# Performance work log

Measured on AMD Instinct MI355X. Metric: run time of the kernel, lower is better.

Reference implementation:

```python
import jax, jax.numpy as jnp
from jax import lax
import numpy as np

HPDF = np.array([-0.0544158422, 0.3128715909, -0.6756307363, 0.5853546837,
                 0.0158291053, -0.284015543, -0.0004724846, 0.1287474266,
                 0.017369301, -0.0440882539, -0.0139810279, 0.008746094,
                 0.004870353, -0.0003917404, -0.0006754494, -0.0001174768],
                dtype=np.float32)


def setup_inputs() -> dict:
    key = jax.random.key(0)
    x = jax.random.normal(key, (8, 3, 512, 512), dtype=jnp.float32)
    hpdf = jnp.asarray(HPDF)
    return {"x": x, "hpdf": hpdf}


def _dwconv(inp, k2d, channels):
    # depthwise valid cross-correlation (matches F.conv2d with groups=C)
    n = k2d.shape[0]
    k = jnp.broadcast_to(k2d[None, None], (channels, 1, n, n))
    return lax.conv_general_dilated(
        inp, k, window_strides=(1, 1), padding='VALID',
        dimension_numbers=('NCHW', 'OIHW', 'NCHW'),
        feature_group_count=channels)


def reference(x, hpdf):
    B, C, H, W = x.shape
    n = hpdf.shape[0]  # 16 taps
    sign = (-1.0) ** jnp.arange(n, dtype=jnp.float32)
    lpdf = sign * hpdf[::-1]
    filters = [jnp.outer(lpdf, hpdf),   # LH
               jnp.outer(hpdf, lpdf),   # HL
               jnp.outer(hpdf, hpdf)]   # HH
    pad = n - 1  # 15
    xp = jnp.pad(x, ((0, 0), (0, 0), (pad, pad), (pad, pad)), mode='reflect')

    xis = []
    for f in filters:
        R = _dwconv(xp, f, C)                       # [B,C,H+15,W+15]
        xi = _dwconv(jnp.abs(R), jnp.abs(f[::-1, ::-1]), C)  # [B,C,H,W]
        # filter side length 16 is even -> roll by 1 on both spatial dims
        xi = jnp.roll(jnp.roll(xi, 1, axis=-1), 1, axis=-2)
        xis.append(xi)

    xi_stack = jnp.stack(xis, axis=0)               # [3,B,C,H,W]
    # p = -1: rho = (sum xi^p)^(-1/p) = sum(1/xi)
    rho = jnp.sum(1.0 / xi_stack, axis=0)
    wet = 1e10
    rho = jnp.minimum(rho, wet)
    rho = jnp.where(jnp.isnan(rho), wet, rho)
    mn = rho.min(axis=(-2, -1), keepdims=True)
    mx = rho.max(axis=(-2, -1), keepdims=True)
    rho = (rho - mn) / (mx - mn + 1e-8)
    score = jax.nn.sigmoid(1.0 - rho)
    return x * score
```

## Files before the change

### kernel.cpp

```cpp
#include <hip/hip_runtime.h>
#include <math.h>

#define IMG   512
#define NIMG  24
#define XST   72
#define TST   104
#define RST   56
#define UST   88
#define UOFF  4480
#define P1SZ  7296
#define TSZ   (48 * TST)

typedef _Float16 v8h __attribute__((ext_vector_type(8)));
typedef float    v4f __attribute__((ext_vector_type(4)));

__device__ __forceinline__ v8h load8(const _Float16* p) {
    union { uint4 u; v8h h; } c;
    c.u = *(const uint4*)p;
    return c.h;
}

__device__ __forceinline__ void store4(_Float16* p, v4f a) {
    union { _Float16 h[4]; uint2 u; } c;
    c.h[0] = (_Float16)a[0]; c.h[1] = (_Float16)a[1];
    c.h[2] = (_Float16)a[2]; c.h[3] = (_Float16)a[3];
    *(uint2*)p = c.u;
}

__device__ __forceinline__ void store4abs(_Float16* p, v4f a) {
    union { _Float16 h[4]; uint2 u; } c;
    c.h[0] = (_Float16)fabsf(a[0]); c.h[1] = (_Float16)fabsf(a[1]);
    c.h[2] = (_Float16)fabsf(a[2]); c.h[3] = (_Float16)fabsf(a[3]);
    *(uint2*)p = c.u;
}

__device__ __forceinline__ unsigned pkrtz(float a, float b) {
    union { __fp16 __attribute__((ext_vector_type(2))) v; unsigned u; } c;
    c.v = __builtin_amdgcn_cvt_pkrtz(a, b);
    return c.u;
}

__device__ __forceinline__ unsigned short f2bf(float f) {
    unsigned b = __float_as_uint(f);
    b = (b + 0x7fffu + ((b >> 16) & 1u)) >> 16;
    return (unsigned short)b;
}

__device__ __forceinline__ int refl(int g) {
    return g < 0 ? -g : (g >= IMG ? 2 * IMG - 2 - g : g);
}

__global__ __launch_bounds__(512, 6) void stego_stage1(
    const float* __restrict__ x, const float* __restrict__ hpdf,
    unsigned short* __restrict__ rho_out, float2* __restrict__ bmm)
{
    __shared__ __align__(16) _Float16 pool1[P1SZ];
    __shared__ __align__(16) _Float16 sTL[TSZ];
    __shared__ __align__(16) _Float16 sTH[TSZ];
    __shared__ __align__(16) _Float16 btab[256];
    __shared__ float red[16];

    const int tid = threadIdx.x;
    const int lane = tid & 63, wid = tid >> 6;
    const int n16 = lane & 15, quad = lane >> 4;
    const int Oj = blockIdx.x * 32, Oi = blockIdx.y * 64, img = blockIdx.z;
    const float* ximg = x + (size_t)img * IMG * IMG;

    if (tid < 256) {
        int mode = tid >> 6, t = tid & 63;
        float v = 0.f;
        if (t >= 16 && t < 32) {
            int tap = t - 16;
            int idx = (mode == 0 || mode == 2) ? tap : 15 - tap;
            float c = hpdf[idx];
            if (mode == 1 && (tap & 1)) c = -c;
            if (mode >= 2) c = fabsf(c);
            v = c;
        }
        btab[tid] = (_Float16)v;
    }

    {
        const int cp2 = tid & 31, row0 = tid >> 5;
        const int c0 = Oj - 15 + 2 * cp2;
        if (Oi >= 15 && Oi <= 433 && Oj >= 15 && Oj <= 463) {
            const float* src = ximg + (size_t)(Oi - 15) * IMG + c0;
            #pragma unroll
            for (int k = 0; k < 6; ++k) {
                int i = row0 + (k << 4);
                unsigned pv = 0;
                if (i < 94) pv = pkrtz(src[(size_t)i * IMG], src[(size_t)i * IMG + 1]);
                *(unsigned*)(pool1 + i * XST + 2 * cp2) = pv;
            }
        } else {
            int gj0 = refl(c0), gj1 = refl(c0 + 1);
            #pragma unroll
            for (int k = 0; k < 6; ++k) {
                int i = row0 + (k << 4);
                unsigned pv = 0;
                if (i < 94) {
                    int gi = refl(Oi - 15 + i);
                    pv = pkrtz(ximg[gi * IMG + gj0], ximg[gi * IMG + gj1]);
                }
                *(unsigned*)(pool1 + i * XST + 2 * cp2) = pv;
            }
        }
    }
    __syncthreads();

    v8h band[4];
    {
        const int boff = 16 + quad * 8 - n16;
        #pragma unroll
        for (int m = 0; m < 4; ++m)
            #pragma unroll
            for (int j = 0; j < 8; ++j)
                band[m][j] = btab[m * 64 + boff + j];
    }

    for (int u = wid; u < 18; u += 8) {
        int mt = u % 6, nt = u / 6;
        int m0 = mt * 16, n0 = nt * 16;
        v8h a = load8(pool1 + (m0 + n16) * XST + n0 + quad * 8);
        v4f z = {0.f, 0.f, 0.f, 0.f};
        v4f cL = __builtin_amdgcn_mfma_f32_16x16x32_f16(a, band[1], z, 0, 0, 0);
        v4f cH = __builtin_amdgcn_mfma_f32_16x16x32_f16(a, band[0], z, 0, 0, 0);
        int off = (n0 + n16) * TST + m0 + quad * 4;
        store4(sTL + off, cL);
        store4(sTH + off, cH);
    }
    __syncthreads();

    float rho[4] = {0.f, 0.f, 0.f, 0.f};
    _Float16* Rb = pool1;
    _Float16* Ub = pool1 + UOFF;

    const int fB[3] = {0, 1, 0};
    const int fC[3] = {2, 3, 3};
    const int fD[3] = {3, 2, 3};

    #pragma unroll
    for (int f = 0; f < 3; ++f) {
        const _Float16* Tsrc = (f == 0) ? sTL : sTH;

        for (int u = wid; u < 15; u += 8) {
            int nt = u % 5, mt = u / 5;
            int i0 = nt * 16, c0 = mt * 16;
            v8h a = load8(Tsrc + (c0 + n16) * TST + i0 + quad * 8);
            v4f z = {0.f, 0.f, 0.f, 0.f};
            v4f acc = __builtin_amdgcn_mfma_f32_16x16x32_f16(a, band[fB[f]], z, 0, 0, 0);
            store4abs(Rb + (i0 + n16) * RST + c0 + quad * 4, acc);
        }
        __syncthreads();

        for (int u = wid; u < 10; u += 8) {
            int mt = u % 5, nt = u / 5;
            int i0 = mt * 16, j0 = nt * 16;
            v8h a = load8(Rb + (i0 + n16) * RST + j0 + quad * 8);
            v4f z = {0.f, 0.f, 0.f, 0.f};
            v4f acc = __builtin_amdgcn_mfma_f32_16x16x32_f16(a, band[fC[f]], z, 0, 0, 0);
            store4(Ub + (j0 + n16) * UST + i0 + quad * 4, acc);
        }
        __syncthreads();

        {
            int i0 = (wid & 3) * 16, c0 = (wid >> 2) * 16;
            v8h a = load8(Ub + (c0 + n16) * UST + i0 + quad * 8);
            v4f z = {0.f, 0.f, 0.f, 0.f};
            v4f acc = __builtin_amdgcn_mfma_f32_16x16x32_f16(a, band[fD[f]], z, 0, 0, 0);
            #pragma unroll
            for (int r = 0; r < 4; ++r) rho[r] += __builtin_amdgcn_rcpf(acc[r]);
        }
    }

    const size_t rbase = (size_t)img * (IMG * IMG);
    const int i_out = (Oi + (wid & 3) * 16 + n16 + 1) & 511;
    const int c0f = (wid >> 2) * 16;
    float lmin = 1e38f, lmax = 0.f;
    #pragma unroll
    for (int r = 0; r < 4; ++r) {
        float v = rho[r];
        v = isnan(v) ? 1e10f : fminf(v, 1e10f);
        unsigned short b = f2bf(v);
        int j_out = (Oj + c0f + quad * 4 + r + 1) & 511;
        rho_out[rbase + ((size_t)i_out << 9) + j_out] = b;
        float rq = __uint_as_float((unsigned)b << 16);
        lmin = fminf(lmin, rq);
        lmax = fmaxf(lmax, rq);
    }
    #pragma unroll
    for (int off = 32; off >= 1; off >>= 1) {
        lmin = fminf(lmin, __shfl_xor(lmin, off));
        lmax = fmaxf(lmax, __shfl_xor(lmax, off));
    }
    if ((tid & 63) == 0) { red[wid] = lmin; red[8 + wid] = lmax; }
    __syncthreads();
    if (tid == 0) {
        float m0 = red[0], m1 = red[8];
        #pragma unroll
        for (int k = 1; k < 8; ++k) { m0 = fminf(m0, red[k]); m1 = fmaxf(m1, red[8 + k]); }
        bmm[(img << 7) + blockIdx.y * 16 + blockIdx.x] = make_float2(m0, m1);
    }
}

__global__ __launch_bounds__(256) void stego_stage2(
    const float* __restrict__ x, const unsigned short* __restrict__ rho,
    const float2* __restrict__ bmm, float* __restrict__ out)
{
    __shared__ float sred[8];
    const int tid = threadIdx.x;
    const int t = blockIdx.x * 256 + tid;
    const int img = t >> 15;

    float lmn = 1e38f, lmx = 0.f;
    if (tid < 128) { float2 p = bmm[(img << 7) + tid]; lmn = p.x; lmx = p.y; }
    #pragma unroll
    for (int off = 32; off >= 1; off >>= 1) {
        lmn = fminf(lmn, __shfl_xor(lmn, off));
        lmx = fmaxf(lmx, __shfl_xor(lmx, off));
    }
    if (tid < 128 && (tid & 63) == 0) { sred[tid >> 6] = lmn; sred[4 + (tid >> 6)] = lmx; }
    __syncthreads();
    const float mn = fminf(sred[0], sred[1]);
    const float mx = fmaxf(sred[4], sred[5]);
    const float inv = __builtin_amdgcn_rcpf(mx - mn + 1e-8f);

    const size_t base = (size_t)t << 3;
    uint4 rb = *(const uint4*)(rho + base);
    unsigned ru[4] = {rb.x, rb.y, rb.z, rb.w};
    float r[8];
    #pragma unroll
    for (int k = 0; k < 4; ++k) {
        r[2 * k]     = __uint_as_float(ru[k] << 16);
        r[2 * k + 1] = __uint_as_float(ru[k] & 0xffff0000u);
    }

    const float* xrow = x + base;
    float4 xa = *(const float4*)xrow;
    float4 xb = *(const float4*)(xrow + 4);
    float xs[8] = {xa.x, xa.y, xa.z, xa.w, xb.x, xb.y, xb.z, xb.w};
    float os[8];
    #pragma unroll
    for (int k = 0; k < 8; ++k) {
        float rn = (r[k] - mn) * inv;
        os[k] = xs[k] * __builtin_amdgcn_rcpf(1.f + __expf(rn - 1.f));
    }
    float* orow = out + base;
    *(float4*)orow       = make_float4(os[0], os[1], os[2], os[3]);
    *(float4*)(orow + 4) = make_float4(os[4], os[5], os[6], os[7]);
}

extern "C" void kernel_launch(void* const* d_in, const int* in_sizes, int n_in,
                              void* d_out, int out_size, void* d_ws, size_t ws_size,
                              hipStream_t stream) {
    const float* x    = (const float*)d_in[0];
    const float* hpdf = (const float*)d_in[1];
    float* out = (float*)d_out;

    unsigned short* rho = (unsigned short*)d_ws;
    float2* bmm = (float2*)((char*)d_ws + (size_t)NIMG * IMG * IMG * 2);

    hipLaunchKernelGGL(stego_stage1, dim3(IMG / 32, IMG / 64, NIMG), dim3(512), 0, stream,
                       x, hpdf, rho, bmm);
    const int total8 = NIMG * IMG * IMG / 8;
    hipLaunchKernelGGL(stego_stage2, dim3(total8 / 256), dim3(256), 0, stream,
                       x, rho, bmm, out);
}
```

Measured before the change: 119.7 us.

## Vectorize tile loads, store rho unrolled, and map images to XCDs

The input tile load now reads float4 per thread with a one-column shift, which is compensated by alternate band coefficient vectors (bandA). Rho is written in natural order as packed 8-byte stores, and the roll by one is moved into stage 2 through a row offset plus a lane shuffle. Both kernels use a 1D grid remapped so each image's blocks land on the same XCD, which should improve L2 locality. The index remapping and shifted filter coefficients are easy to get subtly wrong.

```diff
diff --git a/kernel.cpp b/kernel.cpp
--- a/kernel.cpp
+++ b/kernel.cpp
@@ -20,6 +20,12 @@
     return c.h;
 }
 
+__device__ __forceinline__ unsigned pkrtz(float a, float b) {
+    union { __fp16 __attribute__((ext_vector_type(2))) v; unsigned u; } c;
+    c.v = __builtin_amdgcn_cvt_pkrtz(a, b);
+    return c.u;
+}
+
 __device__ __forceinline__ void store4(_Float16* p, v4f a) {
     union { _Float16 h[4]; uint2 u; } c;
     c.h[0] = (_Float16)a[0]; c.h[1] = (_Float16)a[1];
@@ -32,12 +38,6 @@
     c.h[0] = (_Float16)fabsf(a[0]); c.h[1] = (_Float16)fabsf(a[1]);
     c.h[2] = (_Float16)fabsf(a[2]); c.h[3] = (_Float16)fabsf(a[3]);
     *(uint2*)p = c.u;
-}
-
-__device__ __forceinline__ unsigned pkrtz(float a, float b) {
-    union { __fp16 __attribute__((ext_vector_type(2))) v; unsigned u; } c;
-    c.v = __builtin_amdgcn_cvt_pkrtz(a, b);
-    return c.u;
 }
 
 __device__ __forceinline__ unsigned short f2bf(float f) {
@@ -57,17 +57,25 @@
     __shared__ __align__(16) _Float16 pool1[P1SZ];
     __shared__ __align__(16) _Float16 sTL[TSZ];
     __shared__ __align__(16) _Float16 sTH[TSZ];
-    __shared__ __align__(16) _Float16 btab[256];
+    __shared__ __align__(16) _Float16 btab[512];
     __shared__ float red[16];
 
     const int tid = threadIdx.x;
-    const int lane = tid & 63, wid = tid >> 6;
+    const int lane = tid & 63;
+    const int wid = __builtin_amdgcn_readfirstlane(tid >> 6);
     const int n16 = lane & 15, quad = lane >> 4;
-    const int Oj = blockIdx.x * 32, Oi = blockIdx.y * 64, img = blockIdx.z;
-    const float* ximg = x + (size_t)img * IMG * IMG;
-
-    if (tid < 256) {
-        int mode = tid >> 6, t = tid & 63;
+
+    const int blk = blockIdx.x;
+    const int xcd = blk & 7;
+    const int grp = blk >> 3;
+    const int img = xcd + ((grp >> 7) << 3);
+    const int tl  = grp & 127;
+    const int Oi = (tl >> 4) << 6;
+    const int Oj = (tl & 15) << 5;
+    const float* ximg = x + (size_t)img * (IMG * IMG);
+
+    {
+        const int mode = tid >> 7, t = tid & 127;
         float v = 0.f;
         if (t >= 16 && t < 32) {
             int tap = t - 16;
@@ -81,41 +89,54 @@
     }
 
     {
-        const int cp2 = tid & 31, row0 = tid >> 5;
-        const int c0 = Oj - 15 + 2 * cp2;
-        if (Oi >= 15 && Oi <= 433 && Oj >= 15 && Oj <= 463) {
-            const float* src = ximg + (size_t)(Oi - 15) * IMG + c0;
-            #pragma unroll
-            for (int k = 0; k < 6; ++k) {
-                int i = row0 + (k << 4);
-                unsigned pv = 0;
-                if (i < 94) pv = pkrtz(src[(size_t)i * IMG], src[(size_t)i * IMG + 1]);
-                *(unsigned*)(pool1 + i * XST + 2 * cp2) = pv;
+        const int cg = tid & 15, row0 = tid >> 4;
+        const int c0 = Oj - 16 + 4 * cg;
+        _Float16* dst = pool1 + row0 * XST + 4 * cg;
+        if (Oi >= 15 && Oi <= 433 && Oj >= 16 && Oj <= 464) {
+            const float* src = ximg + (size_t)(Oi - 15 + row0) * IMG + c0;
+            #pragma unroll
+            for (int k = 0; k < 3; ++k) {
+                const int row = row0 + (k << 5);
+                uint2 pv = make_uint2(0u, 0u);
+                if (row < 94) {
+                    float4 xv = *(const float4*)(src + (size_t)(k << 5) * IMG);
+                    pv.x = pkrtz(xv.x, xv.y);
+                    pv.y = pkrtz(xv.z, xv.w);
+                }
+                *(uint2*)(dst + (size_t)(k << 5) * XST) = pv;
             }
         } else {
-            int gj0 = refl(c0), gj1 = refl(c0 + 1);
-            #pragma unroll
-            for (int k = 0; k < 6; ++k) {
-                int i = row0 + (k << 4);
-                unsigned pv = 0;
-                if (i < 94) {
-                    int gi = refl(Oi - 15 + i);
-                    pv = pkrtz(ximg[gi * IMG + gj0], ximg[gi * IMG + gj1]);
+            const int gj0 = refl(c0),     gj1 = refl(c0 + 1);
+            const int gj2 = refl(c0 + 2), gj3 = refl(c0 + 3);
+            #pragma unroll
+            for (int k = 0; k < 3; ++k) {
+                const int row = row0 + (k << 5);
+                uint2 pv = make_uint2(0u, 0u);
+                if (row < 94) {
+                    const float* rsrc = ximg + (size_t)refl(Oi - 15 + row) * IMG;
+                    pv.x = pkrtz(rsrc[gj0], rsrc[gj1]);
+                    pv.y = pkrtz(rsrc[gj2], rsrc[gj3]);
                 }
-                *(unsigned*)(pool1 + i * XST + 2 * cp2) = pv;
+                *(uint2*)(dst + (size_t)(k << 5) * XST) = pv;
             }
         }
     }
     __syncthreads();
 
-    v8h band[4];
+    v8h band[4], bandA[2];
     {
-        const int boff = 16 + quad * 8 - n16;
+        const int boff  = 16 + quad * 8 - n16;
+        const int boffA = 15 + quad * 8 - n16;
         #pragma unroll
         for (int m = 0; m < 4; ++m)
             #pragma unroll
             for (int j = 0; j < 8; ++j)
-                band[m][j] = btab[m * 64 + boff + j];
+                band[m][j] = btab[m * 128 + boff + j];
+        #pragma unroll
+        for (int m = 0; m < 2; ++m)
+            #pragma unroll
+            for (int j = 0; j < 8; ++j)
+                bandA[m][j] = btab[m * 128 + boffA + j];
     }
 
     for (int u = wid; u < 18; u += 8) {
@@ -123,8 +144,8 @@
         int m0 = mt * 16, n0 = nt * 16;
         v8h a = load8(pool1 + (m0 + n16) * XST + n0 + quad * 8);
         v4f z = {0.f, 0.f, 0.f, 0.f};
-        v4f cL = __builtin_amdgcn_mfma_f32_16x16x32_f16(a, band[1], z, 0, 0, 0);
-        v4f cH = __builtin_amdgcn_mfma_f32_16x16x32_f16(a, band[0], z, 0, 0, 0);
+        v4f cL = __builtin_amdgcn_mfma_f32_16x16x32_f16(a, bandA[1], z, 0, 0, 0);
+        v4f cH = __builtin_amdgcn_mfma_f32_16x16x32_f16(a, bandA[0], z, 0, 0, 0);
         int off = (n0 + n16) * TST + m0 + quad * 4;
         store4(sTL + off, cL);
         store4(sTH + off, cH);
@@ -174,20 +195,26 @@
     }
 
     const size_t rbase = (size_t)img * (IMG * IMG);
-    const int i_out = (Oi + (wid & 3) * 16 + n16 + 1) & 511;
-    const int c0f = (wid >> 2) * 16;
+    const int i_nat = Oi + (wid & 3) * 16 + n16;
+    const int jb = Oj + ((wid >> 2) << 4) + quad * 4;
     float lmin = 1e38f, lmax = 0.f;
-    #pragma unroll
-    for (int r = 0; r < 4; ++r) {
-        float v = rho[r];
-        v = isnan(v) ? 1e10f : fminf(v, 1e10f);
-        unsigned short b = f2bf(v);
-        int j_out = (Oj + c0f + quad * 4 + r + 1) & 511;
-        rho_out[rbase + ((size_t)i_out << 9) + j_out] = b;
-        float rq = __uint_as_float((unsigned)b << 16);
-        lmin = fminf(lmin, rq);
-        lmax = fmaxf(lmax, rq);
-    }
+    unsigned pk0, pk1;
+    {
+        unsigned short b[4];
+        #pragma unroll
+        for (int r = 0; r < 4; ++r) {
+            float v = rho[r];
+            v = isnan(v) ? 1e10f : fminf(v, 1e10f);
+            b[r] = f2bf(v);
+            float rq = __uint_as_float((unsigned)b[r] << 16);
+            lmin = fminf(lmin, rq);
+            lmax = fmaxf(lmax, rq);
+        }
+        pk0 = (unsigned)b[0] | ((unsigned)b[1] << 16);
+        pk1 = (unsigned)b[2] | ((unsigned)b[3] << 16);
+    }
+    *(uint2*)(rho_out + rbase + ((size_t)i_nat << 9) + jb) = make_uint2(pk0, pk1);
+
     #pragma unroll
     for (int off = 32; off >= 1; off >>= 1) {
         lmin = fminf(lmin, __shfl_xor(lmin, off));
@@ -199,7 +226,7 @@
         float m0 = red[0], m1 = red[8];
         #pragma unroll
         for (int k = 1; k < 8; ++k) { m0 = fminf(m0, red[k]); m1 = fmaxf(m1, red[8 + k]); }
-        bmm[(img << 7) + blockIdx.y * 16 + blockIdx.x] = make_float2(m0, m1);
+        bmm[(img << 7) + tl] = make_float2(m0, m1);
     }
 }
 
@@ -209,8 +236,13 @@
 {
     __shared__ float sred[8];
     const int tid = threadIdx.x;
-    const int t = blockIdx.x * 256 + tid;
-    const int img = t >> 15;
+    const int lane = tid & 63;
+
+    const int blk = blockIdx.x;
+    const int xcd = blk & 7, grp = blk >> 3;
+    const int img = xcd + ((grp >> 7) << 3);
+    const int chunk = grp & 127;
+    const int t = (img << 15) + (chunk << 8) + tid;
 
     float lmn = 1e38f, lmx = 0.f;
     if (tid < 128) { float2 p = bmm[(img << 7) + tid]; lmn = p.x; lmx = p.y; }
@@ -225,16 +257,23 @@
     const float mx = fmaxf(sred[4], sred[5]);
     const float inv = __builtin_amdgcn_rcpf(mx - mn + 1e-8f);
 
+    const int i = (t >> 6) & 511;
+    const int rrow = (i - 1) & 511;
+    const size_t rb_off = ((size_t)img << 18) + ((size_t)rrow << 9) + ((size_t)lane << 3);
+    uint4 rb = *(const uint4*)(rho + rb_off);
+    unsigned ru[4] = {rb.x, rb.y, rb.z, rb.w};
+    float f7 = __uint_as_float(ru[3] & 0xffff0000u);
+    float r[8];
+    r[0] = __shfl(f7, (lane + 63) & 63);
+    r[1] = __uint_as_float(ru[0] << 16);
+    r[2] = __uint_as_float(ru[0] & 0xffff0000u);
+    r[3] = __uint_as_float(ru[1] << 16);
+    r[4] = __uint_as_float(ru[1] & 0xffff0000u);
+    r[5] = __uint_as_float(ru[2] << 16);
+    r[6] = __uint_as_float(ru[2] & 0xffff0000u);
+    r[7] = __uint_as_float(ru[3] << 16);
+
     const size_t base = (size_t)t << 3;
-    uint4 rb = *(const uint4*)(rho + base);
-    unsigned ru[4] = {rb.x, rb.y, rb.z, rb.w};
-    float r[8];
-    #pragma unroll
-    for (int k = 0; k < 4; ++k) {
-        r[2 * k]     = __uint_as_float(ru[k] << 16);
-        r[2 * k + 1] = __uint_as_float(ru[k] & 0xffff0000u);
-    }
-
     const float* xrow = x + base;
     float4 xa = *(const float4*)xrow;
     float4 xb = *(const float4*)(xrow + 4);
@@ -260,9 +299,8 @@
     unsigned short* rho = (unsigned short*)d_ws;
     float2* bmm = (float2*)((char*)d_ws + (size_t)NIMG * IMG * IMG * 2);
 
-    hipLaunchKernelGGL(stego_stage1, dim3(IMG / 32, IMG / 64, NIMG), dim3(512), 0, stream,
+    hipLaunchKernelGGL(stego_stage1, dim3(NIMG * 128), dim3(512), 0, stream,
                        x, hpdf, rho, bmm);
-    const int total8 = NIMG * IMG * IMG / 8;
-    hipLaunchKernelGGL(stego_stage2, dim3(total8 / 256), dim3(256), 0, stream,
+    hipLaunchKernelGGL(stego_stage2, dim3(NIMG * 128), dim3(256), 0, stream,
                        x, rho, bmm, out);
 }
```

After: 117.7 us. About the same (-1.7%).
